# Performance work log

Hardware: AMD Instinct MI355X
Metric: run time of the kernel (lower is better)

The kernel has to match this reference:

```python
import jax, jax.numpy as jnp
import numpy as np

N = 200000   # num atoms (nodes)
E = 400000   # one-way edges; symmetrized to 2E inside forward
H = 256      # hidden_dim == hidden_feats
LN_EPS = 1e-5


def setup_inputs() -> dict:
    key = jax.random.key(0)
    ks = jax.random.split(key, 48)
    def p(i, shape, s=0.05):
        return jax.random.normal(ks[i], shape, dtype=jnp.float32) * s
    inp = {
        'atom_inputs': jax.random.randint(ks[0], (N, 7), 0, 2),
        'src': jax.random.randint(ks[1], (E,), 0, N),
        'dst': jax.random.randint(ks[2], (E,), 0, N),
        # AtomEmbedding tables
        'emb_element': p(3, (100, 64)),
        'emb_degree': p(4, (7, 4)),
        'emb_valence': p(5, (7, 4)),
        'emb_charge': p(6, (8, 4)),
        'emb_aromatic': p(7, (2, 4)),
        'emb_hybrid': p(8, (6, 4)),
        'emb_hydrogen': p(9, (5, 4)),
        # linear_0: 88 -> H
        'W0': p(10, (88, H)), 'b0': jnp.zeros((H,), jnp.float32),
        # linear_1: H -> H
        'W1': p(11, (H, H)), 'b1': jnp.zeros((H,), jnp.float32),
    }
    # 4 GINEConv layers: node-MLP weight Wn/bn, edge Linear(1,H) weight We/be,
    # followed by LayerNorm gamma g / beta bt
    for i in range(4):
        inp[f'Wn{i}'] = p(12 + 4 * i, (H, H))
        inp[f'bn{i}'] = jnp.zeros((H,), jnp.float32)
        inp[f'We{i}'] = p(13 + 4 * i, (H,))
        inp[f'be{i}'] = jnp.zeros((H,), jnp.float32)
        inp[f'g{i}'] = jnp.ones((H,), jnp.float32)
        inp[f'bt{i}'] = jnp.zeros((H,), jnp.float32)
    return inp


def _layernorm(x, g, b):
    m = jnp.mean(x, axis=-1, keepdims=True)
    v = jnp.mean(jnp.square(x - m), axis=-1, keepdims=True)
    return (x - m) / jnp.sqrt(v + LN_EPS) * g + b


def reference(atom_inputs, src, dst,
              emb_element, emb_degree, emb_valence, emb_charge,
              emb_aromatic, emb_hybrid, emb_hydrogen,
              W0, b0, W1, b1,
              Wn0, bn0, We0, be0, g0, bt0,
              Wn1, bn1, We1, be1, g1, bt1,
              Wn2, bn2, We2, be2, g2, bt2,
              Wn3, bn3, We3, be3, g3, bt3):
    # --- AtomEmbedding: 7 lookups, concat -> [N, 88]
    feats = jnp.concatenate([
        emb_element[atom_inputs[:, 0]],
        emb_degree[atom_inputs[:, 1]],
        emb_valence[atom_inputs[:, 2] + 1],
        emb_charge[atom_inputs[:, 3]],
        emb_aromatic[atom_inputs[:, 4]],
        emb_hybrid[atom_inputs[:, 5]],
        emb_hydrogen[atom_inputs[:, 6]],
    ], axis=-1)
    h = feats @ W0 + b0  # [N, H]
    n = h.shape[0]

    # symmetrize edges: src||dst -> dst||src
    s = jnp.concatenate([src, dst])
    d = jnp.concatenate([dst, src])

    def gine(x, Wn, bn, We, be):
        # edge_attr is all-ones [2E,1]; Linear(1,H) applied to ones is the
        # constant vector We + be broadcast over edges.
        c = We + be                                   # [H]
        msg = jax.nn.relu(x[s] + c)                   # [2E, H] gather + add
        agg = jax.ops.segment_sum(msg, d, num_segments=n)  # scatter-sum
        return (x + agg) @ Wn + bn                    # eps=0: (1+eps)*x + agg

    h = _layernorm(gine(h, Wn0, bn0, We0, be0), g0, bt0)
    h = _layernorm(gine(h, Wn1, bn1, We1, be1), g1, bt1)
    h = _layernorm(gine(h, Wn2, bn2, We2, be2), g2, bt2)
    h = _layernorm(gine(h, Wn3, bn3, We3, be3), g3, bt3)
    return h @ W1 + b1
```

## Files before the change

kernel.cpp:

```cpp
#include <hip/hip_runtime.h>

#define HDIM 256

typedef __attribute__((ext_vector_type(8))) short short8;
typedef __attribute__((ext_vector_type(4))) float f32x4;

typedef const __attribute__((address_space(1))) unsigned int* gas_ptr;
typedef __attribute__((address_space(3))) unsigned int* las_ptr;

__device__ __forceinline__ unsigned short f2bf(float f) {
    unsigned int u = __float_as_uint(f);
    u += 0x7FFF + ((u >> 16) & 1);
    return (unsigned short)(u >> 16);
}
__device__ __forceinline__ float bf2f(unsigned short u) {
    return __uint_as_float(((unsigned int)u) << 16);
}


__global__ void k_zero_int(int* p, int n) {
    int i = blockIdx.x * blockDim.x + threadIdx.x;
    if (i < n) p[i] = 0;
}

__global__ void k_hist(const int* __restrict__ src, const int* __restrict__ dst,
                       int E, int* __restrict__ deg) {
    int e = blockIdx.x * blockDim.x + threadIdx.x;
    if (e >= E) return;
    atomicAdd(&deg[dst[e]], 1);
    atomicAdd(&deg[src[e]], 1);
}

__global__ void k_scan_partial(const int* __restrict__ deg, int* __restrict__ rp,
                               int* __restrict__ bsum, int n) {
    __shared__ int sd[256];
    int t = threadIdx.x;
    int base = blockIdx.x * 1024 + t * 4;
    int v[4]; int tsum = 0;
    #pragma unroll
    for (int k = 0; k < 4; k++) { v[k] = (base + k < n) ? deg[base + k] : 0; tsum += v[k]; }
    sd[t] = tsum; __syncthreads();
    for (int off = 1; off < 256; off <<= 1) {
        int x = (t >= off) ? sd[t - off] : 0;
        __syncthreads();
        sd[t] += x;
        __syncthreads();
    }
    int run = sd[t] - tsum;
    if (t == 255) bsum[blockIdx.x] = sd[255];
    #pragma unroll
    for (int k = 0; k < 4; k++) { if (base + k < n) rp[base + k] = run; run += v[k]; }
}

__global__ void k_scan_bsum(int* __restrict__ bsum, int nb) {
    __shared__ int sd[256];
    int t = threadIdx.x;
    int base = t * 4;
    int v[4]; int tsum = 0;
    #pragma unroll
    for (int k = 0; k < 4; k++) { v[k] = (base + k < nb) ? bsum[base + k] : 0; tsum += v[k]; }
    sd[t] = tsum; __syncthreads();
    for (int off = 1; off < 256; off <<= 1) {
        int x = (t >= off) ? sd[t - off] : 0;
        __syncthreads();
        sd[t] += x;
        __syncthreads();
    }
    int run = sd[t] - tsum;
    #pragma unroll
    for (int k = 0; k < 4; k++) { if (base + k < nb) bsum[base + k] = run; run += v[k]; }
}

__global__ void k_scan_add(int* __restrict__ rp, int* __restrict__ cursor,
                           const int* __restrict__ bsum, int n, int twoE) {
    int i = blockIdx.x * blockDim.x + threadIdx.x;
    if (i < n) {
        int v = rp[i] + bsum[i >> 10];
        rp[i] = v;
        cursor[i] = v;
    }
    if (i == 0) rp[n] = twoE;
}

__global__ void k_fill(const int* __restrict__ src, const int* __restrict__ dst,
                       int E, int* __restrict__ cursor, int* __restrict__ col) {
    int e = blockIdx.x * blockDim.x + threadIdx.x;
    if (e >= E) return;
    int s = src[e], d = dst[e];
    int p = atomicAdd(&cursor[d], 1); col[p] = s;
    int q = atomicAdd(&cursor[s], 1); col[q] = d;
}


__global__ void k_prep_w(const float* __restrict__ W, unsigned short* __restrict__ Wt) {
    int k = blockIdx.x, nn = threadIdx.x;
    Wt[nn * 256 + k] = f2bf(W[k * 256 + nn]);
}

__global__ void k_prep_w0(const float* __restrict__ W0, unsigned short* __restrict__ Wt0) {
    int k = blockIdx.x, nn = threadIdx.x;
    Wt0[nn * 96 + k] = (k < 88) ? f2bf(W0[k * 256 + nn]) : 0;
}


__global__ __launch_bounds__(256) void k_embed0(
    const int* __restrict__ atom,
    const float* __restrict__ eE, const float* __restrict__ eD,
    const float* __restrict__ eV, const float* __restrict__ eC,
    const float* __restrict__ eA, const float* __restrict__ eH,
    const float* __restrict__ eHy,
    const unsigned short* __restrict__ Wt0, const float* __restrict__ b0,
    unsigned short* __restrict__ x, int n) {
    __shared__ __align__(128) unsigned short As[64 * 256];
    int t = threadIdx.x;
    size_t node0 = (size_t)blockIdx.x * 64;

    {
        int row = t >> 2;
        int ks  = (t & 3) * 24;
        size_t node = node0 + row;
        int a0 = 0, a1 = 0, a2 = 0, a3 = 0, a4 = 0, a5 = 0, a6 = 0;
        bool ok = node < (size_t)n;
        if (ok) {
            const int* a = atom + node * 7;
            a0 = a[0]; a1 = a[1]; a2 = a[2]; a3 = a[3]; a4 = a[4]; a5 = a[5]; a6 = a[6];
        }
        #pragma unroll
        for (int kk = 0; kk < 24; kk++) {
            int k = ks + kk;
            float val = 0.f;
            if (ok) {
                if (k < 64)       val = eE[a0 * 64 + k];
                else if (k < 68)  val = eD[a1 * 4 + (k - 64)];
                else if (k < 72)  val = eV[(a2 + 1) * 4 + (k - 68)];
                else if (k < 76)  val = eC[a3 * 4 + (k - 72)];
                else if (k < 80)  val = eA[a4 * 4 + (k - 76)];
                else if (k < 84)  val = eH[a5 * 4 + (k - 80)];
                else if (k < 88)  val = eHy[a6 * 4 + (k - 84)];
            }
            int boff = (k * 2) ^ ((row & 7) << 4);
            *(unsigned short*)((char*)As + row * 256 + boff) = f2bf(val);
        }
    }
    __syncthreads();

    int w  = t >> 6;
    int l  = t & 63;
    int lr = l & 15;
    int lk = l >> 4;

    f32x4 acc[4][4];
    #pragma unroll
    for (int rg = 0; rg < 4; rg++)
        #pragma unroll
        for (int cg = 0; cg < 4; cg++)
            acc[rg][cg] = (f32x4){0.f, 0.f, 0.f, 0.f};

    #pragma unroll
    for (int kt = 0; kt < 3; kt++) {
        int kbyte = kt * 64 + lk * 16;
        short8 a[4], bf[4];
        #pragma unroll
        for (int rg = 0; rg < 4; rg++) {
            int row = rg * 16 + lr;
            a[rg] = *(const short8*)((const char*)As + row * 256 + (kbyte ^ ((row & 7) << 4)));
        }
        #pragma unroll
        for (int cg = 0; cg < 4; cg++) {
            int coln = w * 64 + cg * 16 + lr;
            bf[cg] = *(const short8*)((const char*)Wt0 + coln * 192 + kbyte);
        }
        #pragma unroll
        for (int rg = 0; rg < 4; rg++)
            #pragma unroll
            for (int cg = 0; cg < 4; cg++)
                acc[rg][cg] = __builtin_amdgcn_mfma_f32_16x16x32_bf16(a[rg], bf[cg], acc[rg][cg], 0, 0, 0);
    }

    float bcol[4];
    #pragma unroll
    for (int cg = 0; cg < 4; cg++) bcol[cg] = b0[w * 64 + cg * 16 + lr];

    __syncthreads();
    #pragma unroll
    for (int rg = 0; rg < 4; rg++)
        #pragma unroll
        for (int j = 0; j < 4; j++) {
            int row = rg * 16 + lk * 4 + j;
            #pragma unroll
            for (int cg = 0; cg < 4; cg++) {
                int colI = w * 64 + cg * 16 + lr;
                int byte = row * 512 + ((((colI >> 2) << 3) ^ ((row & 7) << 4)) + (colI & 3) * 2);
                *(unsigned short*)((char*)As + byte) = f2bf(acc[rg][cg][j] + bcol[cg]);
            }
        }
    __syncthreads();
    ushort4* xo = (ushort4*)(x + node0 * HDIM);
    #pragma unroll
    for (int i = 0; i < 16; i++) {
        int g4 = i * 256 + t;
        int row = g4 >> 6, c4 = g4 & 63;
        if (node0 + row < (size_t)n)
            xo[g4] = *(ushort4*)((char*)As + row * 512 + ((c4 << 3) ^ ((row & 7) << 4)));
    }
}


__global__ __launch_bounds__(256) void k_aggregate(
    const unsigned short* __restrict__ x, const int* __restrict__ rp,
    const int* __restrict__ col, const float* __restrict__ We,
    const float* __restrict__ be, unsigned short* __restrict__ z, int n) {
    int wid = threadIdx.x >> 6;
    int l   = threadIdx.x & 63;
    int node = blockIdx.x * 4 + wid;
    if (node >= n) return;
    int h = l >> 5;
    int j = l & 31;
    const short8* x8 = (const short8*)x;

    float c[8];
    {
        float4 w0 = ((const float4*)We)[2 * j],     w1 = ((const float4*)We)[2 * j + 1];
        float4 e0 = ((const float4*)be)[2 * j],     e1 = ((const float4*)be)[2 * j + 1];
        c[0] = w0.x + e0.x; c[1] = w0.y + e0.y; c[2] = w0.z + e0.z; c[3] = w0.w + e0.w;
        c[4] = w1.x + e1.x; c[5] = w1.y + e1.y; c[6] = w1.z + e1.z; c[7] = w1.w + e1.w;
    }

    float acc[8];
    #pragma unroll
    for (int k = 0; k < 8; k++) acc[k] = 0.f;
    if (h == 0) {
        short8 s = x8[(size_t)node * 32 + j];
        #pragma unroll
        for (int k = 0; k < 8; k++) acc[k] = bf2f((unsigned short)s[k]);
    }

    int p0 = rp[node], p1 = rp[node + 1];
    int p = p0 + h;
    for (; p + 2 < p1; p += 4) {
        int s0 = col[p], s1 = col[p + 2];
        short8 u0 = x8[(size_t)s0 * 32 + j];
        short8 u1 = x8[(size_t)s1 * 32 + j];
        #pragma unroll
        for (int k = 0; k < 8; k++) acc[k] += fmaxf(bf2f((unsigned short)u0[k]) + c[k], 0.f);
        #pragma unroll
        for (int k = 0; k < 8; k++) acc[k] += fmaxf(bf2f((unsigned short)u1[k]) + c[k], 0.f);
    }
    for (; p < p1; p += 2) {
        int s0 = col[p];
        short8 u0 = x8[(size_t)s0 * 32 + j];
        #pragma unroll
        for (int k = 0; k < 8; k++) acc[k] += fmaxf(bf2f((unsigned short)u0[k]) + c[k], 0.f);
    }

    #pragma unroll
    for (int k = 0; k < 8; k++) acc[k] += __shfl_xor(acc[k], 32, 64);

    if (h == 0) {
        short8 o;
        #pragma unroll
        for (int k = 0; k < 8; k++) o[k] = (short)f2bf(acc[k]);
        ((short8*)z)[(size_t)node * 32 + j] = o;
    }
}


template <bool DO_LN>
__global__ __launch_bounds__(256) void k_gemm_mfma(
    const unsigned short* __restrict__ zin, const unsigned short* __restrict__ Wt,
    const float* __restrict__ b, const float* __restrict__ g,
    const float* __restrict__ bt, void* __restrict__ xout_v, int n) {
    __shared__ __align__(128) unsigned short As[64 * 256];
    __shared__ float psum[4][64], psq[4][64];
    __shared__ float mean_s[64], inv_s[64];

    int t = threadIdx.x;
    int w = t >> 6;
    int l = t & 63;
    size_t node0 = (size_t)blockIdx.x * 64;

    if (node0 + 64 <= (size_t)n) {
        const char* ztile = (const char*)(zin + node0 * HDIM);
        #pragma unroll
        for (int it = 0; it < 8; it++) {
            int ldsbase = w * 8192 + it * 1024;
            int row = (ldsbase >> 9) + (l >> 5);
            int chunk = (l & 31) * 16;
            const char* src = ztile + row * 512 + (chunk ^ ((row & 7) << 4));
            __builtin_amdgcn_global_load_lds((gas_ptr)src,
                                             (las_ptr)((char*)As + ldsbase),
                                             16, 0, 0);
        }
    } else {
        const ushort4* zr = (const ushort4*)(zin + node0 * HDIM);
        #pragma unroll
        for (int i = 0; i < 16; i++) {
            int g4 = i * 256 + t;
            int row = g4 >> 6, c4 = g4 & 63;
            ushort4 v = make_ushort4(0, 0, 0, 0);
            if (node0 + row < (size_t)n) v = zr[g4];
            *(ushort4*)((char*)As + row * 512 + ((c4 << 3) ^ ((row & 7) << 4))) = v;
        }
    }
    __syncthreads();

    int lr = l & 15;
    int lk = l >> 4;

    f32x4 acc[4][4];
    #pragma unroll
    for (int rg = 0; rg < 4; rg++)
        #pragma unroll
        for (int cg = 0; cg < 4; cg++)
            acc[rg][cg] = (f32x4){0.f, 0.f, 0.f, 0.f};

    #pragma unroll
    for (int kt = 0; kt < 8; kt++) {
        int kbyte = kt * 64 + lk * 16;
        short8 a[4], bf[4];
        #pragma unroll
        for (int rg = 0; rg < 4; rg++) {
            int row = rg * 16 + lr;
            a[rg] = *(const short8*)((const char*)As + row * 512 + (kbyte ^ ((row & 7) << 4)));
        }
        #pragma unroll
        for (int cg = 0; cg < 4; cg++) {
            int coln = w * 64 + cg * 16 + lr;
            bf[cg] = *(const short8*)((const char*)Wt + coln * 512 + kbyte);
        }
        #pragma unroll
        for (int rg = 0; rg < 4; rg++)
            #pragma unroll
            for (int cg = 0; cg < 4; cg++)
                acc[rg][cg] = __builtin_amdgcn_mfma_f32_16x16x32_bf16(a[rg], bf[cg], acc[rg][cg], 0, 0, 0);
    }

    float bcol[4];
    #pragma unroll
    for (int cg = 0; cg < 4; cg++) bcol[cg] = b[w * 64 + cg * 16 + lr];
    #pragma unroll
    for (int rg = 0; rg < 4; rg++)
        #pragma unroll
        for (int cg = 0; cg < 4; cg++)
            #pragma unroll
            for (int j = 0; j < 4; j++) acc[rg][cg][j] += bcol[cg];

    if (!DO_LN) {
        float* xout = (float*)xout_v;
        #pragma unroll
        for (int rg = 0; rg < 4; rg++)
            #pragma unroll
            for (int j = 0; j < 4; j++) {
                int row = rg * 16 + lk * 4 + j;
                size_t node = node0 + row;
                if (node < (size_t)n) {
                    #pragma unroll
                    for (int cg = 0; cg < 4; cg++)
                        xout[node * HDIM + w * 64 + cg * 16 + lr] = acc[rg][cg][j];
                }
            }
        return;
    }

    float sv[4][4], sq[4][4];
    #pragma unroll
    for (int rg = 0; rg < 4; rg++)
        #pragma unroll
        for (int j = 0; j < 4; j++) {
            float s = 0.f, q = 0.f;
            #pragma unroll
            for (int cg = 0; cg < 4; cg++) {
                float v = acc[rg][cg][j];
                s += v; q += v * v;
            }
            sv[rg][j] = s; sq[rg][j] = q;
        }
    #pragma unroll
    for (int off = 1; off < 16; off <<= 1) {
        #pragma unroll
        for (int rg = 0; rg < 4; rg++)
            #pragma unroll
            for (int j = 0; j < 4; j++) {
                sv[rg][j] += __shfl_xor(sv[rg][j], off, 64);
                sq[rg][j] += __shfl_xor(sq[rg][j], off, 64);
            }
    }
    if (lr == 0) {
        #pragma unroll
        for (int rg = 0; rg < 4; rg++)
            #pragma unroll
            for (int j = 0; j < 4; j++) {
                int row = rg * 16 + lk * 4 + j;
                psum[w][row] = sv[rg][j];
                psq[w][row]  = sq[rg][j];
            }
    }
    __syncthreads();
    if (t < 64) {
        float s = psum[0][t] + psum[1][t] + psum[2][t] + psum[3][t];
        float q = psq[0][t] + psq[1][t] + psq[2][t] + psq[3][t];
        float m = s * (1.f / 256.f);
        float var = q * (1.f / 256.f) - m * m;
        mean_s[t] = m;
        inv_s[t]  = rsqrtf(var + 1e-5f);
    }
    __syncthreads();

    float gv[4], btv[4];
    #pragma unroll
    for (int cg = 0; cg < 4; cg++) {
        int coln = w * 64 + cg * 16 + lr;
        gv[cg] = g[coln]; btv[cg] = bt[coln];
    }
    #pragma unroll
    for (int rg = 0; rg < 4; rg++)
        #pragma unroll
        for (int j = 0; j < 4; j++) {
            int row = rg * 16 + lk * 4 + j;
            float m = mean_s[row];
            float inv = inv_s[row];
            #pragma unroll
            for (int cg = 0; cg < 4; cg++) {
                int colI = w * 64 + cg * 16 + lr;
                float v = (acc[rg][cg][j] - m) * inv * gv[cg] + btv[cg];
                int byte = row * 512 + ((((colI >> 2) << 3) ^ ((row & 7) << 4)) + (colI & 3) * 2);
                *(unsigned short*)((char*)As + byte) = f2bf(v);
            }
        }
    __syncthreads();
    ushort4* xo = (ushort4*)((unsigned short*)xout_v + node0 * HDIM);
    #pragma unroll
    for (int i = 0; i < 16; i++) {
        int g4 = i * 256 + t;
        int row = g4 >> 6, c4 = g4 & 63;
        if (node0 + row < (size_t)n)
            xo[g4] = *(ushort4*)((char*)As + row * 512 + ((c4 << 3) ^ ((row & 7) << 4)));
    }
}


extern "C" void kernel_launch(void* const* d_in, const int* in_sizes, int n_in,
                              void* d_out, int out_size, void* d_ws, size_t ws_size,
                              hipStream_t stream) {
    const int*   atom = (const int*)d_in[0];
    const int*   src  = (const int*)d_in[1];
    const int*   dst  = (const int*)d_in[2];
    const float* eE   = (const float*)d_in[3];
    const float* eD   = (const float*)d_in[4];
    const float* eV   = (const float*)d_in[5];
    const float* eC   = (const float*)d_in[6];
    const float* eA   = (const float*)d_in[7];
    const float* eH   = (const float*)d_in[8];
    const float* eHy  = (const float*)d_in[9];
    const float* W0   = (const float*)d_in[10];
    const float* b0   = (const float*)d_in[11];
    const float* W1   = (const float*)d_in[12];
    const float* b1   = (const float*)d_in[13];

    const int N = in_sizes[0] / 7;
    const int E = in_sizes[1];
    const int twoE = 2 * E;

    unsigned short* xb = (unsigned short*)d_ws;
    unsigned short* z  = xb + (size_t)N * HDIM;
    int*   rp      = (int*)(z + (size_t)N * HDIM);
    int*   cursor  = rp + (N + 1);
    int*   deg     = cursor + N;
    int*   col     = deg + N;
    int*   bsum    = col + twoE;
    uintptr_t pw = (uintptr_t)(bsum + 1024);
    pw = (pw + 255) & ~(uintptr_t)255;
    unsigned short* Wt  = (unsigned short*)pw;
    unsigned short* Wt0 = Wt + (size_t)5 * 65536;

    const int nb = (N + 1023) / 1024;

    k_zero_int<<<(N + 255) / 256, 256, 0, stream>>>(deg, N);
    k_hist<<<(E + 255) / 256, 256, 0, stream>>>(src, dst, E, deg);
    k_scan_partial<<<nb, 256, 0, stream>>>(deg, rp, bsum, N);
    k_scan_bsum<<<1, 256, 0, stream>>>(bsum, nb);
    k_scan_add<<<(N + 255) / 256, 256, 0, stream>>>(rp, cursor, bsum, N, twoE);
    k_fill<<<(E + 255) / 256, 256, 0, stream>>>(src, dst, E, cursor, col);

    for (int L = 0; L < 4; L++) {
        const float* Wn = (const float*)d_in[14 + 6 * L + 0];
        k_prep_w<<<256, 256, 0, stream>>>(Wn, Wt + (size_t)L * 65536);
    }
    k_prep_w<<<256, 256, 0, stream>>>(W1, Wt + (size_t)4 * 65536);
    k_prep_w0<<<96, 256, 0, stream>>>(W0, Wt0);

    const int nblk64 = (N + 63) / 64;
    const int nblk4  = (N + 3) / 4;

    k_embed0<<<nblk64, 256, 0, stream>>>(atom, eE, eD, eV, eC, eA, eH, eHy,
                                         Wt0, b0, xb, N);

    for (int L = 0; L < 4; L++) {
        const float* bn = (const float*)d_in[14 + 6 * L + 1];
        const float* We = (const float*)d_in[14 + 6 * L + 2];
        const float* be = (const float*)d_in[14 + 6 * L + 3];
        const float* g  = (const float*)d_in[14 + 6 * L + 4];
        const float* bt = (const float*)d_in[14 + 6 * L + 5];
        k_aggregate<<<nblk4, 256, 0, stream>>>(xb, rp, col, We, be, z, N);
        k_gemm_mfma<true><<<nblk64, 256, 0, stream>>>(z, Wt + (size_t)L * 65536,
                                                      bn, g, bt, xb, N);
    }

    k_gemm_mfma<false><<<nblk64, 256, 0, stream>>>(xb, Wt + (size_t)4 * 65536,
                                                   b1, nullptr, nullptr, d_out, N);
}
```

Measured before the change: 973.8 us.

## Assign one node per half-wave in aggregation with shuffled neighbor indices

The aggregation kernel now gives each half-wavefront (32 lanes) its own destination node, so one wave handles two nodes instead of splitting one node's edges across halves. The cross-half shuffle reduction goes away. Neighbor indices are loaded cooperatively, 32 at a time, and broadcast with shuffles instead of being loaded per iteration by every lane. This removes the reduction and the redundant index loads, at the cost of divergence when the two nodes in a wave have different degrees.

```diff
diff --git a/kernel.cpp b/kernel.cpp
--- a/kernel.cpp
+++ b/kernel.cpp
@@ -212,10 +212,11 @@
     const float* __restrict__ be, unsigned short* __restrict__ z, int n) {
     int wid = threadIdx.x >> 6;
     int l   = threadIdx.x & 63;
-    int node = blockIdx.x * 4 + wid;
-    if (node >= n) return;
-    int h = l >> 5;
-    int j = l & 31;
+    int h   = l >> 5;
+    int j   = l & 31;
+    int node = blockIdx.x * 8 + wid * 2 + h;
+    bool ok = node < n;
+    int nd = ok ? node : 0;
     const short8* x8 = (const short8*)x;
 
     float c[8];
@@ -226,41 +227,43 @@
         c[4] = w1.x + e1.x; c[5] = w1.y + e1.y; c[6] = w1.z + e1.z; c[7] = w1.w + e1.w;
     }
 
+    int p0 = rp[nd], p1 = rp[nd + 1];
+    int deg = ok ? (p1 - p0) : 0;
+
     float acc[8];
-    #pragma unroll
-    for (int k = 0; k < 8; k++) acc[k] = 0.f;
-    if (h == 0) {
-        short8 s = x8[(size_t)node * 32 + j];
-        #pragma unroll
-        for (int k = 0; k < 8; k++) acc[k] = bf2f((unsigned short)s[k]);
-    }
-
-    int p0 = rp[node], p1 = rp[node + 1];
-    int p = p0 + h;
-    for (; p + 2 < p1; p += 4) {
-        int s0 = col[p], s1 = col[p + 2];
-        short8 u0 = x8[(size_t)s0 * 32 + j];
-        short8 u1 = x8[(size_t)s1 * 32 + j];
-        #pragma unroll
-        for (int k = 0; k < 8; k++) acc[k] += fmaxf(bf2f((unsigned short)u0[k]) + c[k], 0.f);
-        #pragma unroll
-        for (int k = 0; k < 8; k++) acc[k] += fmaxf(bf2f((unsigned short)u1[k]) + c[k], 0.f);
-    }
-    for (; p < p1; p += 2) {
-        int s0 = col[p];
-        short8 u0 = x8[(size_t)s0 * 32 + j];
-        #pragma unroll
-        for (int k = 0; k < 8; k++) acc[k] += fmaxf(bf2f((unsigned short)u0[k]) + c[k], 0.f);
-    }
-
-    #pragma unroll
-    for (int k = 0; k < 8; k++) acc[k] += __shfl_xor(acc[k], 32, 64);
-
-    if (h == 0) {
+    {
+        short8 s = x8[(size_t)nd * 32 + j];
+        #pragma unroll
+        for (int k = 0; k < 8; k++) acc[k] = ok ? bf2f((unsigned short)s[k]) : 0.f;
+    }
+
+    for (int b = 0; b < deg; b += 32) {
+        int m = deg - b; if (m > 32) m = 32;
+        int idx = (j < m) ? col[p0 + b + j] : 0;
+        int e = 0;
+        for (; e + 2 <= m; e += 2) {
+            int s0 = __shfl(idx, (h << 5) + e, 64);
+            int s1 = __shfl(idx, (h << 5) + e + 1, 64);
+            short8 u0 = x8[(size_t)s0 * 32 + j];
+            short8 u1 = x8[(size_t)s1 * 32 + j];
+            #pragma unroll
+            for (int k = 0; k < 8; k++) acc[k] += fmaxf(bf2f((unsigned short)u0[k]) + c[k], 0.f);
+            #pragma unroll
+            for (int k = 0; k < 8; k++) acc[k] += fmaxf(bf2f((unsigned short)u1[k]) + c[k], 0.f);
+        }
+        if (e < m) {
+            int s0 = __shfl(idx, (h << 5) + e, 64);
+            short8 u0 = x8[(size_t)s0 * 32 + j];
+            #pragma unroll
+            for (int k = 0; k < 8; k++) acc[k] += fmaxf(bf2f((unsigned short)u0[k]) + c[k], 0.f);
+        }
+    }
+
+    if (ok) {
         short8 o;
         #pragma unroll
         for (int k = 0; k < 8; k++) o[k] = (short)f2bf(acc[k]);
-        ((short8*)z)[(size_t)node * 32 + j] = o;
+        ((short8*)z)[(size_t)nd * 32 + j] = o;
     }
 }
 
@@ -490,7 +493,7 @@
     k_prep_w0<<<96, 256, 0, stream>>>(W0, Wt0);
 
     const int nblk64 = (N + 63) / 64;
-    const int nblk4  = (N + 3) / 4;
+    const int nblk8  = (N + 7) / 8;
 
     k_embed0<<<nblk64, 256, 0, stream>>>(atom, eE, eD, eV, eC, eA, eH, eHy,
                                          Wt0, b0, xb, N);
@@ -501,7 +504,7 @@
         const float* be = (const float*)d_in[14 + 6 * L + 3];
         const float* g  = (const float*)d_in[14 + 6 * L + 4];
         const float* bt = (const float*)d_in[14 + 6 * L + 5];
-        k_aggregate<<<nblk4, 256, 0, stream>>>(xb, rp, col, We, be, z, N);
+        k_aggregate<<<nblk8, 256, 0, stream>>>(xb, rp, col, We, be, z, N);
         k_gemm_mfma<true><<<nblk64, 256, 0, stream>>>(z, Wt + (size_t)L * 65536,
                                                       bn, g, bt, xb, N);
     }
```

After: 936.7 us. -3.8%, faster.
